# Kernel tuning notes

Hardware: AMD Instinct MI355X
Metric: run time of the kernel (lower is better)

The kernel has to match this reference:

```python
import jax, jax.numpy as jnp
import numpy as np

N_NODES = 50000


def setup_inputs() -> dict:
    key = jax.random.key(0)
    k1, k2, k3, k4 = jax.random.split(key, 4)
    N, E, D_IN, D_OUT = N_NODES, 1_600_000, 128, 128
    x = jax.random.normal(k1, (N, D_IN), dtype=jnp.float32)
    edge_index = jax.random.randint(k2, (2, E), 0, N, dtype=jnp.int64)
    W = jax.random.normal(k3, (D_IN, D_OUT), dtype=jnp.float32) * (1.0 / np.sqrt(D_IN))
    b = jax.random.normal(k4, (D_OUT,), dtype=jnp.float32) * 0.01
    return {"x": x, "edge_index": edge_index, "W": W, "b": b}


def reference(x, edge_index, W, b):
    N = x.shape[0]
    # add self loops: edge (i, i) for every node
    loops = jnp.arange(N, dtype=edge_index.dtype)
    row = jnp.concatenate([edge_index[0], loops])  # [E+N]
    col = jnp.concatenate([edge_index[1], loops])  # [E+N]
    # degree over col (matches torch_geometric degree(col, N))
    deg = jax.ops.segment_sum(jnp.ones_like(col, dtype=x.dtype), col, num_segments=N)
    deg_inv_sqrt = jnp.where(deg > 0, jax.lax.rsqrt(jnp.maximum(deg, 1.0)), 0.0)
    norm = deg_inv_sqrt[row] * deg_inv_sqrt[col]  # [E+N]
    # linear transform then gather-multiply-scatter (segment sum over row)
    xl = x @ W + b  # [N, D_OUT]
    msg = norm[:, None] * xl[col]  # [E+N, D_OUT]
    out = jax.ops.segment_sum(msg, row, num_segments=N)
    return out
```

## Files before the change

kernel.cpp:

```cpp
#include <hip/hip_runtime.h>
#include <hip/hip_bf16.h>


#define D     128
#define TILE  8192
#define BINB  1024
#define RPB   64
#define CAPB  4096
#define MAXBK 1024
#define NH    256

typedef short  bf16x8 __attribute__((ext_vector_type(8)));
typedef float  f32x4  __attribute__((ext_vector_type(4)));
typedef unsigned short us4 __attribute__((ext_vector_type(4)));
typedef unsigned short us8 __attribute__((ext_vector_type(8)));

static __device__ __forceinline__ unsigned short f2bf(float f) {
    unsigned u = __float_as_uint(f);
    u = (u + 0x7FFFu + ((u >> 16) & 1u)) >> 16;
    return (unsigned short)u;
}
static __device__ __forceinline__ float bf2f(unsigned short s) {
    return __uint_as_float(((unsigned)s) << 16);
}

__global__ __launch_bounds__(256) void k_prep(const float* __restrict__ W,
                                              unsigned short* __restrict__ wtb,
                                              int* __restrict__ bcur,
                                              int NBK) {
    int i = blockIdx.x * 256 + threadIdx.x;
    if (i < NBK) bcur[i] = i * CAPB;
    if (i < D * D) {
        int n = i >> 7, k = i & 127;
        wtb[n * 128 + k] = f2bf(W[k * 128 + n]);
    }
}

__global__ __launch_bounds__(1024) void k_hist(const int* __restrict__ cols,
                                               unsigned* __restrict__ phist,
                                               int E, int NW) {
    __shared__ unsigned hist[16384];
    const int t = threadIdx.x;
    for (int w = t; w < NW; w += 1024) hist[w] = 0;
    __syncthreads();
    const int hb   = blockIdx.x;
    const int SEG  = (E + NH - 1) / NH;
    const int hbeg = hb * SEG;
    int hend = hbeg + SEG; if (hend > E) hend = E;
    for (int i = hbeg + t; i < hend; i += 1024) {
        unsigned c = (unsigned)cols[i];
        atomicAdd(&hist[c >> 2], 1u << ((c & 3u) * 8u));
    }
    __syncthreads();
    unsigned* dst = phist + (size_t)hb * NW;
    for (int w = t; w < NW; w += 1024) dst[w] = hist[w];
}

__global__ __launch_bounds__(256) void k_dismerge(const unsigned* __restrict__ phist,
                                                  float* __restrict__ dis,
                                                  int N, int NW) {
    int w = blockIdx.x * 256 + threadIdx.x;
    if (w >= NW) return;
    unsigned s0 = 0, s1 = 0, s2 = 0, s3 = 0;
    const unsigned* pw = phist + w;
    #pragma unroll 8
    for (int b = 0; b < NH; ++b) {
        unsigned u = pw[(size_t)b * NW];
        s0 += u & 255u;
        s1 += (u >> 8) & 255u;
        s2 += (u >> 16) & 255u;
        s3 += u >> 24;
    }
    int c0 = w * 4;
    float4 o = make_float4(rsqrtf((float)(s0 + 1)), rsqrtf((float)(s1 + 1)),
                           rsqrtf((float)(s2 + 1)), rsqrtf((float)(s3 + 1)));
    if (c0 + 3 < N) {
        *(float4*)&dis[c0] = o;
    } else {
        if (c0     < N) dis[c0]     = o.x;
        if (c0 + 1 < N) dis[c0 + 1] = o.y;
        if (c0 + 2 < N) dis[c0 + 2] = o.z;
        if (c0 + 3 < N) dis[c0 + 3] = o.w;
    }
}

__global__ __launch_bounds__(1024) void k_gemm(
        const float* __restrict__ x, const unsigned short* __restrict__ wtb,
        const float* __restrict__ bia, const float* __restrict__ dis,
        unsigned short* __restrict__ xlb, int N) {
    __shared__ __align__(16) unsigned char smem[52224];
    unsigned short (*wt)[136] = (unsigned short (*)[136])smem;
    unsigned short (*xs)[136] = (unsigned short (*)[136])(smem + 34816);
    unsigned short (*ys)[128] = (unsigned short (*)[128])smem;
    const int t = threadIdx.x;
    const int row0 = blockIdx.x * 64;
    #pragma unroll
    for (int i = 0; i < 2; ++i) {
        int j = i * 1024 + t;
        int n = j >> 4, k8 = j & 15;
        us8 v = *(const us8*)&wtb[j * 8];
        *(us8*)&wt[n][k8 * 8] = v;
    }
    #pragma unroll
    for (int i = 0; i < 2; ++i) {
        int j = i * 1024 + t;
        int r = j >> 5, c4 = j & 31;
        int gr = row0 + r;
        us4 o = (us4){0, 0, 0, 0};
        if (gr < N) {
            float4 v = *(const float4*)&x[(size_t)gr * D + c4 * 4];
            o = (us4){f2bf(v.x), f2bf(v.y), f2bf(v.z), f2bf(v.w)};
        }
        *(us4*)&xs[r][c4 * 4] = o;
    }
    __syncthreads();
    f32x4 acc[8];
    if (t < 256) {
        const int w  = t >> 6, l = t & 63;
        const int m0 = w * 16;
        const int lm = l & 15, lq = l >> 4;
        #pragma unroll
        for (int nt = 0; nt < 8; ++nt) acc[nt] = (f32x4){0.f, 0.f, 0.f, 0.f};
        #pragma unroll
        for (int kk = 0; kk < 4; ++kk) {
            const int kof = kk * 32 + lq * 8;
            bf16x8 a = *(const bf16x8*)&xs[m0 + lm][kof];
            #pragma unroll
            for (int nt = 0; nt < 8; ++nt) {
                bf16x8 bb = *(const bf16x8*)&wt[nt * 16 + lm][kof];
                acc[nt] = __builtin_amdgcn_mfma_f32_16x16x32_bf16(a, bb, acc[nt], 0, 0, 0);
            }
        }
    }
    __syncthreads();
    if (t < 256) {
        const int w  = t >> 6, l = t & 63;
        const int m0 = w * 16;
        const int lm = l & 15, lq = l >> 4;
        float bc[8];
        #pragma unroll
        for (int nt = 0; nt < 8; ++nt) bc[nt] = bia[nt * 16 + lm];
        #pragma unroll
        for (int r = 0; r < 4; ++r) {
            int lrow = m0 + lq * 4 + r;
            int grow = row0 + lrow;
            float dv = (grow < N) ? dis[grow] : 0.0f;
            #pragma unroll
            for (int nt = 0; nt < 8; ++nt)
                ys[lrow][nt * 16 + lm] = f2bf(dv * (acc[nt][r] + bc[nt]));
        }
    }
    __syncthreads();
    {
        int r = t >> 4, e8 = t & 15;
        int grow = row0 + r;
        if (grow < N)
            *(us8*)&xlb[(size_t)grow * D + e8 * 8] = *(const us8*)&ys[r][e8 * 8];
    }
}

__global__ __launch_bounds__(1024) void k_bin(
        const int* __restrict__ rows, const int* __restrict__ cols,
        int* __restrict__ bcur, unsigned* __restrict__ ebuf,
        int E, int NBK) {
    __shared__ __align__(16) unsigned char smem[45568];
    unsigned* sorted = (unsigned*)smem;
    int* lcnt  = (int*)(smem + 32768);
    int* lbase = lcnt + 800;
    int* excl  = lcnt + 1600;
    int* cur   = lcnt + 2400;
    const int t = threadIdx.x;

    const int base = blockIdx.x * TILE;
    int m = E - base; if (m > TILE) m = TILE;

    unsigned p[TILE / BINB];
    #pragma unroll
    for (int it = 0; it < TILE / BINB; ++it) {
        int i = it * BINB + t;
        if (i < m) {
            unsigned r = (unsigned)rows[base + i];
            unsigned c = (unsigned)cols[base + i];
            p[it] = c | ((r & 63u) << 16) | ((r >> 6) << 22);
        }
    }
    if (t < 800) lcnt[t] = 0;
    __syncthreads();
    #pragma unroll
    for (int it = 0; it < TILE / BINB; ++it) {
        int i = it * BINB + t;
        if (i < m) atomicAdd(&lcnt[p[it] >> 22], 1);
    }
    __syncthreads();
    if (t < 64) {
        int v[13], s = 0;
        #pragma unroll
        for (int u = 0; u < 13; ++u) {
            int k = t * 13 + u;
            v[u] = (k < NBK) ? lcnt[k] : 0;
            s += v[u];
        }
        int inc = s;
        #pragma unroll
        for (int off = 1; off < 64; off <<= 1) { int o = __shfl_up(inc, off); if (t >= off) inc += o; }
        int run = inc - s;
        #pragma unroll
        for (int u = 0; u < 13; ++u) {
            int k = t * 13 + u;
            if (k < NBK) { excl[k] = run; cur[k] = run; }
            run += v[u];
        }
    }
    if (t < NBK) {
        int tb = t + (int)((blockIdx.x * 331u) % (unsigned)NBK);
        if (tb >= NBK) tb -= NBK;
        int c0 = lcnt[tb];
        lbase[tb] = c0 ? atomicAdd(&bcur[tb], c0) : 0;
    }
    __syncthreads();
    #pragma unroll
    for (int it = 0; it < TILE / BINB; ++it) {
        int i = it * BINB + t;
        if (i < m) {
            int pos = atomicAdd(&cur[p[it] >> 22], 1);
            sorted[pos] = p[it];
        }
    }
    __syncthreads();
    #pragma unroll
    for (int it = 0; it < TILE / BINB; ++it) {
        int i = it * BINB + t;
        if (i < m) {
            unsigned pp = sorted[i];
            int bk = pp >> 22;
            int g  = lbase[bk] + i - excl[bk];
            if (g < (bk + 1) * CAPB) ebuf[g] = pp & 0x3FFFFFu;
        }
    }
}

__global__ __launch_bounds__(512) void k_sortred4(
        const int* __restrict__ bcur, const unsigned* __restrict__ ebuf,
        const float* __restrict__ dis, const unsigned short* __restrict__ xlb,
        float* __restrict__ out, int N) {
    __shared__ unsigned short sorted[CAPB];
    __shared__ int cnt[RPB];
    __shared__ int excl[RPB];
    __shared__ int cur[RPB];
    const int t = threadIdx.x, b = blockIdx.x;
    const int ebase = b * CAPB;
    int mb = bcur[b] - ebase;
    if (mb > CAPB) mb = CAPB;
    if (mb < 0) mb = 0;

    if (t < RPB) cnt[t] = 0;
    __syncthreads();
    for (int i = t; i < mb; i += 512)
        atomicAdd(&cnt[(ebuf[ebase + i] >> 16) & 63], 1);
    __syncthreads();
    if (t < 64) {
        int v = cnt[t], inc = v;
        #pragma unroll
        for (int off = 1; off < 64; off <<= 1) { int o = __shfl_up(inc, off); if (t >= off) inc += o; }
        excl[t] = inc - v;
        cur[t]  = inc - v;
    }
    __syncthreads();
    for (int i = t; i < mb; i += 512) {
        unsigned pp = ebuf[ebase + i];
        int pos = atomicAdd(&cur[(pp >> 16) & 63], 1);
        sorted[pos] = (unsigned short)(pp & 0xFFFFu);
    }
    __syncthreads();

    const int wv = t >> 6, lane = t & 63;
    const int half = lane >> 5, l32 = lane & 31;

#define FETCH(V, J) do { \
    _Pragma("unroll") \
    for (int u = 0; u < 8; ++u) { \
        int cc = __shfl(c, (J) + 2 * u + half); \
        V[u] = *(const us4*)&xlb[((size_t)cc << 7) + (l32 << 2)]; \
    } } while (0)
#define CFULL(V) do { \
    _Pragma("unroll") \
    for (int u = 0; u < 8; ++u) { \
        a0 += bf2f(V[u][0]); a1 += bf2f(V[u][1]); \
        a2 += bf2f(V[u][2]); a3 += bf2f(V[u][3]); \
    } } while (0)
#define CTAIL(V, J) do { \
    _Pragma("unroll") \
    for (int u = 0; u < 8; ++u) { \
        float w = ((J) + 2 * u + half < mm) ? 1.0f : 0.0f; \
        a0 = fmaf(w, bf2f(V[u][0]), a0); a1 = fmaf(w, bf2f(V[u][1]), a1); \
        a2 = fmaf(w, bf2f(V[u][2]), a2); a3 = fmaf(w, bf2f(V[u][3]), a3); \
    } } while (0)

    for (int r8 = 0; r8 < 8; ++r8) {
        const int rl = wv * 8 + r8;
        const int grow = b * RPB + rl;
        if (grow >= N) break;
        const int beg = excl[rl], end = cur[rl];
        us4 sv = *(const us4*)&xlb[(size_t)grow * D + (l32 << 2)];
        float s = (half == 0) ? 1.0f : 0.0f;
        float a0 = s * bf2f(sv[0]), a1 = s * bf2f(sv[1]);
        float a2 = s * bf2f(sv[2]), a3 = s * bf2f(sv[3]);
        for (int bs = beg; bs < end; bs += 64) {
            int mm = end - bs; if (mm > 64) mm = 64;
            int c = 0;
            if (lane < mm) c = sorted[bs + lane];
            us4 A[8], B[8];
            int j = 0;
            FETCH(A, 0);
            for (; j + 32 <= mm; j += 32) {
                FETCH(B, j + 16);
                CFULL(A);
                if (j + 32 < mm) FETCH(A, j + 32);
                CFULL(B);
            }
            int rem = mm - j;
            if (rem > 0) {
                if (rem > 16) { FETCH(B, j + 16); CFULL(A); CTAIL(B, j + 16); }
                else          { CTAIL(A, j); }
            }
        }
        a0 += __shfl_xor(a0, 32);
        a1 += __shfl_xor(a1, 32);
        a2 += __shfl_xor(a2, 32);
        a3 += __shfl_xor(a3, 32);
        if (half == 0) {
            const float di = dis[grow];
            *(float4*)&out[(size_t)grow * D + (l32 << 2)] =
                make_float4(di * a0, di * a1, di * a2, di * a3);
        }
    }
#undef FETCH
#undef CFULL
#undef CTAIL
}

__global__ __launch_bounds__(256) void k_zero(int* __restrict__ p, int n) {
    int i = blockIdx.x * 256 + threadIdx.x;
    if (i < n) p[i] = 0;
}
__global__ __launch_bounds__(256) void k_deg(const int* __restrict__ cols,
                                             int* __restrict__ cntc, int E) {
    int e = blockIdx.x * 256 + threadIdx.x;
    if (e < E) atomicAdd(&cntc[cols[e]], 1);
}
__global__ __launch_bounds__(256) void k_dis(const int* __restrict__ cntc,
                                             float* __restrict__ dis, int N) {
    int i = blockIdx.x * 256 + threadIdx.x;
    if (i < N) dis[i] = rsqrtf((float)(cntc[i] + 1));
}
#define GEMM_R 8
__global__ __launch_bounds__(128) void k_gemmf(const float* __restrict__ x,
                                               const float* __restrict__ W,
                                               const float* __restrict__ b,
                                               float* __restrict__ xl, int N) {
    __shared__ float xs[GEMM_R][D];
    const int c  = threadIdx.x;
    const int r0 = blockIdx.x * GEMM_R;
    #pragma unroll
    for (int r = 0; r < GEMM_R; ++r) {
        int row = r0 + r;
        xs[r][c] = (row < N) ? x[row * D + c] : 0.0f;
    }
    __syncthreads();
    float acc[GEMM_R];
    const float bc = b[c];
    #pragma unroll
    for (int r = 0; r < GEMM_R; ++r) acc[r] = bc;
    for (int k = 0; k < D; k += 4) {
        const float w0 = W[(k + 0) * D + c];
        const float w1 = W[(k + 1) * D + c];
        const float w2 = W[(k + 2) * D + c];
        const float w3 = W[(k + 3) * D + c];
        #pragma unroll
        for (int r = 0; r < GEMM_R; ++r) {
            const float4 xv = *reinterpret_cast<const float4*>(&xs[r][k]);
            acc[r] = fmaf(xv.x, w0, acc[r]);
            acc[r] = fmaf(xv.y, w1, acc[r]);
            acc[r] = fmaf(xv.z, w2, acc[r]);
            acc[r] = fmaf(xv.w, w3, acc[r]);
        }
    }
    #pragma unroll
    for (int r = 0; r < GEMM_R; ++r) {
        int row = r0 + r;
        if (row < N) xl[row * D + c] = acc[r];
    }
}
__global__ __launch_bounds__(256) void k_self(const float* __restrict__ xl,
                                              const float* __restrict__ dis,
                                              float* __restrict__ out, int N) {
    int gid = blockIdx.x * 256 + threadIdx.x;
    int i = gid >> 7;
    if (i < N) {
        float d = dis[i];
        out[gid] = d * d * xl[gid];
    }
}
__global__ __launch_bounds__(256) void k_scatter(const int* __restrict__ rows,
                                                 const int* __restrict__ cols,
                                                 const float* __restrict__ dis,
                                                 const float* __restrict__ xl,
                                                 float* __restrict__ out, int E) {
    long long gid = (long long)blockIdx.x * 256 + threadIdx.x;
    int e    = (int)(gid >> 6);
    int lane = (int)(gid & 63);
    if (e >= E) return;
    const int row = rows[e];
    const int col = cols[e];
    const float nrm = dis[row] * dis[col];
    atomicAdd(&out[row * D + lane],      nrm * xl[col * D + lane]);
    atomicAdd(&out[row * D + 64 + lane], nrm * xl[col * D + 64 + lane]);
}

extern "C" void kernel_launch(void* const* d_in, const int* in_sizes, int n_in,
                              void* d_out, int out_size, void* d_ws, size_t ws_size,
                              hipStream_t stream) {
    const float* x   = (const float*)d_in[0];
    const int*   ei  = (const int*)d_in[1];
    const float* W   = (const float*)d_in[2];
    const float* b   = (const float*)d_in[3];
    float*       out = (float*)d_out;

    const int N = in_sizes[0] / D;
    const int E = in_sizes[1] / 2;
    const int* rows = ei;
    const int* cols = ei + E;
    const int NBK = (N + RPB - 1) / RPB;
    const int NT  = (E + TILE - 1) / TILE;
    const int GN  = (N + 63) / 64;
    const int NW  = (N + 3) / 4;

    char* p = (char*)d_ws;
    size_t off = 0;
    unsigned short* xlb     = (unsigned short*)(p + off); off += (size_t)N * D * 2;
    unsigned short* wtb     = (unsigned short*)(p + off); off += (size_t)D * D * 2;
    float*          dis     = (float*)(p + off);          off += (size_t)N * 4;
    int*            bcur    = (int*)(p + off);            off += (size_t)MAXBK * 4;
    unsigned*       ebuf    = (unsigned*)(p + off);       off += (size_t)NBK * CAPB * 4;
    unsigned*       phist   = (unsigned*)(p + off);       off += (size_t)NH * NW * 4;

    const int gN = (N + 255) / 256;
    const int gE = (E + 255) / 256;

    if (N <= 65536 && NBK <= 800 && ws_size >= off) {
        int gP = (D * D + 255) / 256;
        if (gP < (NBK + 255) / 256) gP = (NBK + 255) / 256;
        k_prep     <<<gP, 256, 0, stream>>>(W, wtb, bcur, NBK);
        k_hist     <<<NH, 1024, 0, stream>>>(cols, phist, E, NW);
        k_dismerge <<<(NW + 255) / 256, 256, 0, stream>>>(phist, dis, N, NW);
        k_bin      <<<NT, BINB, 0, stream>>>(rows, cols, bcur, ebuf, E, NBK);
        k_gemm     <<<GN, 1024, 0, stream>>>(x, wtb, b, dis, xlb, N);
        k_sortred4 <<<NBK, 512, 0, stream>>>(bcur, ebuf, dis, xlb, out, N);
    } else {
        char* q = (char*)d_ws;
        float* xl   = (float*)q;
        float* disF = (float*)(q + (size_t)N * D * 4);
        int*   cc   = (int*)(q + (size_t)N * D * 4 + (size_t)N * 4);
        k_zero <<<gN, 256, 0, stream>>>(cc, N);
        k_deg  <<<gE, 256, 0, stream>>>(cols, cc, E);
        k_dis  <<<gN, 256, 0, stream>>>(cc, disF, N);
        k_gemmf<<<(N + GEMM_R - 1) / GEMM_R, 128, 0, stream>>>(x, W, b, xl, N);
        k_self <<<((N * D) + 255) / 256, 256, 0, stream>>>(xl, disF, out, N);
        long long st = (long long)E * 64;
        k_scatter<<<(int)((st + 255) / 256), 256, 0, stream>>>(rows, cols, disF, xl, out, E);
    }
}
```

Baseline: 185.0 us.

## Merge histogram, binning and GEMM into one heterogeneous launch

Combines the column histogram, edge binning and bf16 GEMM kernels into a single launch, with block-index ranges picking the role. This lets the three independent stages overlap on the GPU instead of running back to back. Because the GEMM no longer waits for the degree values, the dis scaling moves into a new elementwise pass over xlb. That pass adds an extra read and write of the N×128 bf16 buffer and a second bf16 rounding. The shared allocation grows to 64 KB for every block, which may lower occupancy for the binning and GEMM roles.

After: 181.4 us. Within noise of the previous version (-1.9%).

```diff
diff --git a/kernel.cpp b/kernel.cpp
--- a/kernel.cpp
+++ b/kernel.cpp
@@ -7,7 +7,6 @@
 #define BINB  1024
 #define RPB   64
 #define CAPB  4096
-#define MAXBK 1024
 #define NH    256
 
 typedef short  bf16x8 __attribute__((ext_vector_type(8)));
@@ -36,24 +35,175 @@
     }
 }
 
-__global__ __launch_bounds__(1024) void k_hist(const int* __restrict__ cols,
-                                               unsigned* __restrict__ phist,
-                                               int E, int NW) {
-    __shared__ unsigned hist[16384];
+__global__ __launch_bounds__(1024) void k_trijoint(
+        const int* __restrict__ rows, const int* __restrict__ cols,
+        int* __restrict__ bcur, unsigned* __restrict__ ebuf,
+        const float* __restrict__ x, const unsigned short* __restrict__ wtb,
+        const float* __restrict__ bia, unsigned short* __restrict__ xlb,
+        unsigned* __restrict__ phist,
+        int E, int N, int NBK, int NT, int GN, int NW) {
+    __shared__ __align__(16) unsigned char smem[65536];
     const int t = threadIdx.x;
-    for (int w = t; w < NW; w += 1024) hist[w] = 0;
-    __syncthreads();
-    const int hb   = blockIdx.x;
-    const int SEG  = (E + NH - 1) / NH;
-    const int hbeg = hb * SEG;
-    int hend = hbeg + SEG; if (hend > E) hend = E;
-    for (int i = hbeg + t; i < hend; i += 1024) {
-        unsigned c = (unsigned)cols[i];
-        atomicAdd(&hist[c >> 2], 1u << ((c & 3u) * 8u));
-    }
-    __syncthreads();
-    unsigned* dst = phist + (size_t)hb * NW;
-    for (int w = t; w < NW; w += 1024) dst[w] = hist[w];
+
+    if ((int)blockIdx.x >= NT + GN) {
+        unsigned* hist = (unsigned*)smem;
+        for (int w = t; w < NW; w += BINB) hist[w] = 0;
+        __syncthreads();
+        const int hb   = (int)blockIdx.x - NT - GN;
+        const int SEG  = (E + NH - 1) / NH;
+        const int hbeg = hb * SEG;
+        int hend = hbeg + SEG; if (hend > E) hend = E;
+        for (int i = hbeg + t; i < hend; i += BINB) {
+            unsigned c = (unsigned)cols[i];
+            atomicAdd(&hist[c >> 2], 1u << ((c & 3u) * 8u));
+        }
+        __syncthreads();
+        unsigned* dst = phist + (size_t)hb * NW;
+        for (int w = t; w < NW; w += BINB) dst[w] = hist[w];
+        return;
+    }
+
+    if ((int)blockIdx.x >= NT) {
+        unsigned short (*wt)[136] = (unsigned short (*)[136])smem;
+        unsigned short (*xs)[136] = (unsigned short (*)[136])(smem + 34816);
+        unsigned short (*ys)[128] = (unsigned short (*)[128])smem;
+        const int row0 = ((int)blockIdx.x - NT) * 64;
+        #pragma unroll
+        for (int i = 0; i < 2; ++i) {
+            int j = i * 1024 + t;
+            int n = j >> 4, k8 = j & 15;
+            us8 v = *(const us8*)&wtb[j * 8];
+            *(us8*)&wt[n][k8 * 8] = v;
+        }
+        #pragma unroll
+        for (int i = 0; i < 2; ++i) {
+            int j = i * 1024 + t;
+            int r = j >> 5, c4 = j & 31;
+            int gr = row0 + r;
+            us4 o = (us4){0, 0, 0, 0};
+            if (gr < N) {
+                float4 v = *(const float4*)&x[(size_t)gr * D + c4 * 4];
+                o = (us4){f2bf(v.x), f2bf(v.y), f2bf(v.z), f2bf(v.w)};
+            }
+            *(us4*)&xs[r][c4 * 4] = o;
+        }
+        __syncthreads();
+        f32x4 acc[8];
+        if (t < 256) {
+            const int w  = t >> 6, l = t & 63;
+            const int m0 = w * 16;
+            const int lm = l & 15, lq = l >> 4;
+            #pragma unroll
+            for (int nt = 0; nt < 8; ++nt) acc[nt] = (f32x4){0.f, 0.f, 0.f, 0.f};
+            #pragma unroll
+            for (int kk = 0; kk < 4; ++kk) {
+                const int kof = kk * 32 + lq * 8;
+                bf16x8 a = *(const bf16x8*)&xs[m0 + lm][kof];
+                #pragma unroll
+                for (int nt = 0; nt < 8; ++nt) {
+                    bf16x8 bb = *(const bf16x8*)&wt[nt * 16 + lm][kof];
+                    acc[nt] = __builtin_amdgcn_mfma_f32_16x16x32_bf16(a, bb, acc[nt], 0, 0, 0);
+                }
+            }
+        }
+        __syncthreads();
+        if (t < 256) {
+            const int w  = t >> 6, l = t & 63;
+            const int m0 = w * 16;
+            const int lm = l & 15, lq = l >> 4;
+            float bc[8];
+            #pragma unroll
+            for (int nt = 0; nt < 8; ++nt) bc[nt] = bia[nt * 16 + lm];
+            #pragma unroll
+            for (int r = 0; r < 4; ++r) {
+                int lrow = m0 + lq * 4 + r;
+                #pragma unroll
+                for (int nt = 0; nt < 8; ++nt)
+                    ys[lrow][nt * 16 + lm] = f2bf(acc[nt][r] + bc[nt]);
+            }
+        }
+        __syncthreads();
+        {
+            int r = t >> 4, e8 = t & 15;
+            int grow = row0 + r;
+            if (grow < N)
+                *(us8*)&xlb[(size_t)grow * D + e8 * 8] = *(const us8*)&ys[r][e8 * 8];
+        }
+        return;
+    }
+
+    unsigned* sorted = (unsigned*)smem;
+    int* lcnt  = (int*)(smem + 32768);
+    int* lbase = lcnt + 800;
+    int* excl  = lcnt + 1600;
+    int* cur   = lcnt + 2400;
+
+    const int base = blockIdx.x * TILE;
+    int m = E - base; if (m > TILE) m = TILE;
+
+    unsigned p[TILE / BINB];
+    #pragma unroll
+    for (int it = 0; it < TILE / BINB; ++it) {
+        int i = it * BINB + t;
+        if (i < m) {
+            unsigned r = (unsigned)rows[base + i];
+            unsigned c = (unsigned)cols[base + i];
+            p[it] = c | ((r & 63u) << 16) | ((r >> 6) << 22);
+        }
+    }
+    if (t < 800) lcnt[t] = 0;
+    __syncthreads();
+    #pragma unroll
+    for (int it = 0; it < TILE / BINB; ++it) {
+        int i = it * BINB + t;
+        if (i < m) atomicAdd(&lcnt[p[it] >> 22], 1);
+    }
+    __syncthreads();
+    if (t < 64) {
+        int v[13], s = 0;
+        #pragma unroll
+        for (int u = 0; u < 13; ++u) {
+            int k = t * 13 + u;
+            v[u] = (k < NBK) ? lcnt[k] : 0;
+            s += v[u];
+        }
+        int inc = s;
+        #pragma unroll
+        for (int off = 1; off < 64; off <<= 1) { int o = __shfl_up(inc, off); if (t >= off) inc += o; }
+        int run = inc - s;
+        #pragma unroll
+        for (int u = 0; u < 13; ++u) {
+            int k = t * 13 + u;
+            if (k < NBK) { excl[k] = run; cur[k] = run; }
+            run += v[u];
+        }
+    }
+    if (t < NBK) {
+        int tb = t + (int)((blockIdx.x * 331u) % (unsigned)NBK);
+        if (tb >= NBK) tb -= NBK;
+        int c0 = lcnt[tb];
+        lbase[tb] = c0 ? atomicAdd(&bcur[tb], c0) : 0;
+    }
+    __syncthreads();
+    #pragma unroll
+    for (int it = 0; it < TILE / BINB; ++it) {
+        int i = it * BINB + t;
+        if (i < m) {
+            int pos = atomicAdd(&cur[p[it] >> 22], 1);
+            sorted[pos] = p[it];
+        }
+    }
+    __syncthreads();
+    #pragma unroll
+    for (int it = 0; it < TILE / BINB; ++it) {
+        int i = it * BINB + t;
+        if (i < m) {
+            unsigned pp = sorted[i];
+            int bk = pp >> 22;
+            int g  = lbase[bk] + i - excl[bk];
+            if (g < (bk + 1) * CAPB) ebuf[g] = pp & 0x3FFFFFu;
+        }
+    }
 }
 
 __global__ __launch_bounds__(256) void k_dismerge(const unsigned* __restrict__ phist,
@@ -84,159 +234,18 @@
     }
 }
 
-__global__ __launch_bounds__(1024) void k_gemm(
-        const float* __restrict__ x, const unsigned short* __restrict__ wtb,
-        const float* __restrict__ bia, const float* __restrict__ dis,
-        unsigned short* __restrict__ xlb, int N) {
-    __shared__ __align__(16) unsigned char smem[52224];
-    unsigned short (*wt)[136] = (unsigned short (*)[136])smem;
-    unsigned short (*xs)[136] = (unsigned short (*)[136])(smem + 34816);
-    unsigned short (*ys)[128] = (unsigned short (*)[128])smem;
-    const int t = threadIdx.x;
-    const int row0 = blockIdx.x * 64;
-    #pragma unroll
-    for (int i = 0; i < 2; ++i) {
-        int j = i * 1024 + t;
-        int n = j >> 4, k8 = j & 15;
-        us8 v = *(const us8*)&wtb[j * 8];
-        *(us8*)&wt[n][k8 * 8] = v;
-    }
-    #pragma unroll
-    for (int i = 0; i < 2; ++i) {
-        int j = i * 1024 + t;
-        int r = j >> 5, c4 = j & 31;
-        int gr = row0 + r;
-        us4 o = (us4){0, 0, 0, 0};
-        if (gr < N) {
-            float4 v = *(const float4*)&x[(size_t)gr * D + c4 * 4];
-            o = (us4){f2bf(v.x), f2bf(v.y), f2bf(v.z), f2bf(v.w)};
-        }
-        *(us4*)&xs[r][c4 * 4] = o;
-    }
-    __syncthreads();
-    f32x4 acc[8];
-    if (t < 256) {
-        const int w  = t >> 6, l = t & 63;
-        const int m0 = w * 16;
-        const int lm = l & 15, lq = l >> 4;
-        #pragma unroll
-        for (int nt = 0; nt < 8; ++nt) acc[nt] = (f32x4){0.f, 0.f, 0.f, 0.f};
-        #pragma unroll
-        for (int kk = 0; kk < 4; ++kk) {
-            const int kof = kk * 32 + lq * 8;
-            bf16x8 a = *(const bf16x8*)&xs[m0 + lm][kof];
-            #pragma unroll
-            for (int nt = 0; nt < 8; ++nt) {
-                bf16x8 bb = *(const bf16x8*)&wt[nt * 16 + lm][kof];
-                acc[nt] = __builtin_amdgcn_mfma_f32_16x16x32_bf16(a, bb, acc[nt], 0, 0, 0);
-            }
-        }
-    }
-    __syncthreads();
-    if (t < 256) {
-        const int w  = t >> 6, l = t & 63;
-        const int m0 = w * 16;
-        const int lm = l & 15, lq = l >> 4;
-        float bc[8];
-        #pragma unroll
-        for (int nt = 0; nt < 8; ++nt) bc[nt] = bia[nt * 16 + lm];
-        #pragma unroll
-        for (int r = 0; r < 4; ++r) {
-            int lrow = m0 + lq * 4 + r;
-            int grow = row0 + lrow;
-            float dv = (grow < N) ? dis[grow] : 0.0f;
-            #pragma unroll
-            for (int nt = 0; nt < 8; ++nt)
-                ys[lrow][nt * 16 + lm] = f2bf(dv * (acc[nt][r] + bc[nt]));
-        }
-    }
-    __syncthreads();
-    {
-        int r = t >> 4, e8 = t & 15;
-        int grow = row0 + r;
-        if (grow < N)
-            *(us8*)&xlb[(size_t)grow * D + e8 * 8] = *(const us8*)&ys[r][e8 * 8];
-    }
-}
-
-__global__ __launch_bounds__(1024) void k_bin(
-        const int* __restrict__ rows, const int* __restrict__ cols,
-        int* __restrict__ bcur, unsigned* __restrict__ ebuf,
-        int E, int NBK) {
-    __shared__ __align__(16) unsigned char smem[45568];
-    unsigned* sorted = (unsigned*)smem;
-    int* lcnt  = (int*)(smem + 32768);
-    int* lbase = lcnt + 800;
-    int* excl  = lcnt + 1600;
-    int* cur   = lcnt + 2400;
-    const int t = threadIdx.x;
-
-    const int base = blockIdx.x * TILE;
-    int m = E - base; if (m > TILE) m = TILE;
-
-    unsigned p[TILE / BINB];
-    #pragma unroll
-    for (int it = 0; it < TILE / BINB; ++it) {
-        int i = it * BINB + t;
-        if (i < m) {
-            unsigned r = (unsigned)rows[base + i];
-            unsigned c = (unsigned)cols[base + i];
-            p[it] = c | ((r & 63u) << 16) | ((r >> 6) << 22);
-        }
-    }
-    if (t < 800) lcnt[t] = 0;
-    __syncthreads();
-    #pragma unroll
-    for (int it = 0; it < TILE / BINB; ++it) {
-        int i = it * BINB + t;
-        if (i < m) atomicAdd(&lcnt[p[it] >> 22], 1);
-    }
-    __syncthreads();
-    if (t < 64) {
-        int v[13], s = 0;
-        #pragma unroll
-        for (int u = 0; u < 13; ++u) {
-            int k = t * 13 + u;
-            v[u] = (k < NBK) ? lcnt[k] : 0;
-            s += v[u];
-        }
-        int inc = s;
-        #pragma unroll
-        for (int off = 1; off < 64; off <<= 1) { int o = __shfl_up(inc, off); if (t >= off) inc += o; }
-        int run = inc - s;
-        #pragma unroll
-        for (int u = 0; u < 13; ++u) {
-            int k = t * 13 + u;
-            if (k < NBK) { excl[k] = run; cur[k] = run; }
-            run += v[u];
-        }
-    }
-    if (t < NBK) {
-        int tb = t + (int)((blockIdx.x * 331u) % (unsigned)NBK);
-        if (tb >= NBK) tb -= NBK;
-        int c0 = lcnt[tb];
-        lbase[tb] = c0 ? atomicAdd(&bcur[tb], c0) : 0;
-    }
-    __syncthreads();
-    #pragma unroll
-    for (int it = 0; it < TILE / BINB; ++it) {
-        int i = it * BINB + t;
-        if (i < m) {
-            int pos = atomicAdd(&cur[p[it] >> 22], 1);
-            sorted[pos] = p[it];
-        }
-    }
-    __syncthreads();
-    #pragma unroll
-    for (int it = 0; it < TILE / BINB; ++it) {
-        int i = it * BINB + t;
-        if (i < m) {
-            unsigned pp = sorted[i];
-            int bk = pp >> 22;
-            int g  = lbase[bk] + i - excl[bk];
-            if (g < (bk + 1) * CAPB) ebuf[g] = pp & 0x3FFFFFu;
-        }
-    }
+__global__ __launch_bounds__(256) void k_disy(const float* __restrict__ dis,
+                                              unsigned short* __restrict__ xlb,
+                                              int N) {
+    int i = blockIdx.x * 256 + threadIdx.x;
+    if (i >= N * (D / 8)) return;
+    int row = i >> 4;
+    float dv = dis[row];
+    us8 v = *(const us8*)&xlb[(size_t)i * 8];
+    us8 o;
+    #pragma unroll
+    for (int k = 0; k < 8; ++k) o[k] = f2bf(dv * bf2f(v[k]));
+    *(us8*)&xlb[(size_t)i * 8] = o;
 }
 
 __global__ __launch_bounds__(512) void k_sortred4(
@@ -440,22 +449,23 @@
     unsigned short* xlb     = (unsigned short*)(p + off); off += (size_t)N * D * 2;
     unsigned short* wtb     = (unsigned short*)(p + off); off += (size_t)D * D * 2;
     float*          dis     = (float*)(p + off);          off += (size_t)N * 4;
-    int*            bcur    = (int*)(p + off);            off += (size_t)MAXBK * 4;
+    int*            bcur    = (int*)(p + off);            off += (size_t)NBK * 4;
     unsigned*       ebuf    = (unsigned*)(p + off);       off += (size_t)NBK * CAPB * 4;
     unsigned*       phist   = (unsigned*)(p + off);       off += (size_t)NH * NW * 4;
 
     const int gN = (N + 255) / 256;
     const int gE = (E + 255) / 256;
 
-    if (N <= 65536 && NBK <= 800 && ws_size >= off) {
+    if (N <= 65536 && NBK <= 800 && NW <= 16384 && ws_size >= off) {
         int gP = (D * D + 255) / 256;
         if (gP < (NBK + 255) / 256) gP = (NBK + 255) / 256;
-        k_prep     <<<gP, 256, 0, stream>>>(W, wtb, bcur, NBK);
-        k_hist     <<<NH, 1024, 0, stream>>>(cols, phist, E, NW);
-        k_dismerge <<<(NW + 255) / 256, 256, 0, stream>>>(phist, dis, N, NW);
-        k_bin      <<<NT, BINB, 0, stream>>>(rows, cols, bcur, ebuf, E, NBK);
-        k_gemm     <<<GN, 1024, 0, stream>>>(x, wtb, b, dis, xlb, N);
-        k_sortred4 <<<NBK, 512, 0, stream>>>(bcur, ebuf, dis, xlb, out, N);
+        k_prep    <<<gP, 256, 0, stream>>>(W, wtb, bcur, NBK);
+        k_trijoint<<<NT + GN + NH, BINB, 0, stream>>>(rows, cols, bcur, ebuf,
+                                                      x, wtb, b, xlb, phist,
+                                                      E, N, NBK, NT, GN, NW);
+        k_dismerge<<<(NW + 255) / 256, 256, 0, stream>>>(phist, dis, N, NW);
+        k_disy    <<<(N * (D / 8) + 255) / 256, 256, 0, stream>>>(dis, xlb, N);
+        k_sortred4<<<NBK, 512, 0, stream>>>(bcur, ebuf, dis, xlb, out, N);
     } else {
         char* q = (char*)d_ws;
         float* xl   = (float*)q;
```
